# Optimization experiments

Measured on AMD Instinct MI355X. Metric: run time of the kernel, lower is better.

The kernel has to match this reference:

```python
import jax, jax.numpy as jnp
import numpy as np

S, I, IN_DIM, PROJ_DIM, OUT_DIM = 128, 384, 256, 32, 128
LN_EPS = 1e-5


def _layer_norm(x):
    # utils.normalize in OmegaFold: F.layer_norm over last dim, no affine params
    mu = jnp.mean(x, axis=-1, keepdims=True)
    var = jnp.var(x, axis=-1, keepdims=True)
    return (x - mu) * jax.lax.rsqrt(var + LN_EPS)


def setup_inputs() -> dict:
    key = jax.random.key(0)
    k0, k1, k2, k3 = jax.random.split(key, 4)
    node_repr = jax.random.normal(k0, (S, I, IN_DIM), dtype=jnp.float32)
    mask = (jax.random.uniform(k1, (S, I)) < 0.9).astype(jnp.float32)
    W_proj = jax.random.normal(k2, (IN_DIM, 2 * PROJ_DIM), dtype=jnp.float32) / np.sqrt(IN_DIM)
    b_proj = jnp.zeros((2 * PROJ_DIM,), dtype=jnp.float32)
    out_weights = jax.random.normal(k3, (PROJ_DIM, PROJ_DIM, OUT_DIM), dtype=jnp.float32) * 0.02
    out_bias = jnp.zeros((OUT_DIM,), dtype=jnp.float32)
    return {
        "node_repr": node_repr,
        "mask": mask,
        "W_proj": W_proj,
        "b_proj": b_proj,
        "out_weights": out_weights,
        "out_bias": out_bias,
    }


def reference(node_repr, mask, W_proj, b_proj, out_weights, out_bias):
    # LayerNorm (no affine) -> linear projection to 2*proj_dim
    x = _layer_norm(node_repr)                       # [s, i, in_dim]
    act = x @ W_proj + b_proj                        # [s, i, 2d]
    m = mask[..., None]                              # [s, i, 1]
    act = act * m
    # mask-pair counts: einsum('si,sj->ij')
    norm = jnp.einsum("si,sj->ij", mask, mask)[..., None]  # [i, j, 1]
    l = act[..., :PROJ_DIM]                          # [s, i, d]
    r = act[..., PROJ_DIM:]                          # [s, j, e]
    # outer-product mean over s, then contract (d,e)->f with the 3-tensor
    outer = jnp.einsum("sid,sje->ijde", l, r)        # [i, j, d, e]
    out = jnp.einsum("ijde,def->ijf", outer, out_weights) + out_bias  # [i, j, f]
    return out / (norm + 0.001)
```

## Files before the change

kernel.cpp:

```cpp
#include <hip/hip_runtime.h>

#define S_DIM 128
#define I_DIM 384
#define IN_DIM 256
#define PD 32
#define ODIM 128

typedef __attribute__((ext_vector_type(8))) __bf16 bf16x8;
typedef __attribute__((ext_vector_type(4))) float f32x4;

#define MFMA16(a, b, c) __builtin_amdgcn_mfma_f32_16x16x32_bf16((a), (b), (c), 0, 0, 0)

__device__ inline unsigned short f2bf(float f) {
    unsigned int u = __builtin_bit_cast(unsigned int, f);
    unsigned int r = (u + 0x7FFFu + ((u >> 16) & 1u)) >> 16;
    return (unsigned short)r;
}

__global__ void prep_cast(const float* __restrict__ Wp, const float* __restrict__ W2,
                          unsigned short* __restrict__ WpT, unsigned short* __restrict__ W2t) {
    int t = blockIdx.x * 256 + threadIdx.x;
    if (t < 64 * 256) {
        int f = t >> 8, k = t & 255;
        WpT[t] = f2bf(Wp[k * 64 + f]);
    }
    if (t < 128 * 1024) {
        int f = t >> 10, de = t & 1023;
        int e = de >> 5, d = de & 31;
        W2t[t] = f2bf(W2[(d * 32 + e) * 128 + f]);
    }
}

__global__ void norm_kernel(const float* __restrict__ mask, float* __restrict__ invn) {
    __shared__ float mi[S_DIM][16];
    __shared__ float mj[S_DIM][16];
    int t = threadIdx.x;
    int i0 = blockIdx.y * 16, j0 = blockIdx.x * 16;
    for (int p = 0; p < 8; ++p) {
        int s = p * 16 + (t >> 4);
        int c = t & 15;
        mi[s][c] = mask[s * I_DIM + i0 + c];
        mj[s][c] = mask[s * I_DIM + j0 + c];
    }
    __syncthreads();
    int ii = t >> 4, jj = t & 15;
    float acc = 0.f;
#pragma unroll 8
    for (int s = 0; s < S_DIM; ++s) acc += mi[s][ii] * mj[s][jj];
    invn[(i0 + ii) * I_DIM + (j0 + jj)] = 1.0f / (acc + 0.001f);
}

__global__ __launch_bounds__(256, 2) void ln_proj(const float* __restrict__ x,
                                                  const float* __restrict__ mask,
                                                  const float* __restrict__ bias,
                                                  const unsigned short* __restrict__ WpT_g,
                                                  unsigned short* __restrict__ lT,
                                                  unsigned short* __restrict__ rT) {
    __shared__ unsigned short xsh[64 * 264];
    __shared__ unsigned short wpT[64 * 264];
    int t = threadIdx.x;
    int w = t >> 6, lane = t & 63;
    int i = blockIdx.x >> 1;
    int s0 = (blockIdx.x & 1) * 64;

    {
        int f = t >> 2, kq = (t & 3) * 64;
#pragma unroll
        for (int p = 0; p < 8; ++p) {
            int k = kq + p * 8;
            *(uint4*)&wpT[f * 264 + k] = *(const uint4*)&WpT_g[f * 256 + k];
        }
    }

    float4 vbuf[4];
#pragma unroll
    for (int p = 0; p < 4; ++p)
        vbuf[p] = *(const float4*)(x + ((size_t)(s0 + w * 16 + p) * I_DIM + i) * IN_DIM + lane * 4);

    for (int it = 0; it < 16; ++it) {
        float4 v = vbuf[it & 3];
        if (it + 4 < 16)
            vbuf[it & 3] = *(const float4*)(x + ((size_t)(s0 + w * 16 + it + 4) * I_DIM + i) * IN_DIM + lane * 4);
        float s1 = v.x + v.y + v.z + v.w;
        float s2 = v.x * v.x + v.y * v.y + v.z * v.z + v.w * v.w;
#pragma unroll
        for (int off = 32; off >= 1; off >>= 1) {
            s1 += __shfl_xor(s1, off);
            s2 += __shfl_xor(s2, off);
        }
        float mu = s1 * (1.f / 256.f);
        float var = s2 * (1.f / 256.f) - mu * mu;
        float rs = rsqrtf(var + 1e-5f);
        unsigned int h0 = f2bf((v.x - mu) * rs);
        unsigned int h1 = f2bf((v.y - mu) * rs);
        unsigned int h2 = f2bf((v.z - mu) * rs);
        unsigned int h3 = f2bf((v.w - mu) * rs);
        uint2 pk;
        pk.x = h0 | (h1 << 16);
        pk.y = h2 | (h3 << 16);
        *(uint2*)&xsh[(w * 16 + it) * 264 + lane * 4] = pk;
    }
    __syncthreads();

    int l15 = lane & 15, q = lane >> 4;
    f32x4 acc[4];
#pragma unroll
    for (int nt = 0; nt < 4; ++nt) acc[nt] = (f32x4){0.f, 0.f, 0.f, 0.f};

    for (int k0 = 0; k0 < 256; k0 += 32) {
        bf16x8 a = *(bf16x8*)&xsh[(w * 16 + l15) * 264 + k0 + q * 8];
#pragma unroll
        for (int nt = 0; nt < 4; ++nt) {
            bf16x8 b = *(bf16x8*)&wpT[(nt * 16 + l15) * 264 + k0 + q * 8];
            acc[nt] = MFMA16(a, b, acc[nt]);
        }
    }

    float mval[4];
#pragma unroll
    for (int reg = 0; reg < 4; ++reg)
        mval[reg] = mask[(size_t)(s0 + w * 16 + q * 4 + reg) * I_DIM + i];

    __syncthreads();
    unsigned short* trsh = xsh;

#pragma unroll
    for (int nt = 0; nt < 4; ++nt) {
        int f = nt * 16 + l15;
        float bv = bias[f];
        unsigned int lo = (unsigned int)f2bf((acc[nt][0] + bv) * mval[0]) |
                          ((unsigned int)f2bf((acc[nt][1] + bv) * mval[1]) << 16);
        unsigned int hi = (unsigned int)f2bf((acc[nt][2] + bv) * mval[2]) |
                          ((unsigned int)f2bf((acc[nt][3] + bv) * mval[3]) << 16);
        uint2 pk; pk.x = lo; pk.y = hi;
        *(uint2*)&trsh[f * 72 + w * 16 + q * 4] = pk;
    }
    __syncthreads();

    {
        int fr = t >> 2, so = (t & 3) * 16;
        unsigned short* dst = ((fr < 32) ? lT : rT) + ((size_t)(i * 32 + (fr & 31)) * 128 + s0 + so);
        *(uint4*)dst = *(uint4*)&trsh[fr * 72 + so];
        *(uint4*)(dst + 8) = *(uint4*)&trsh[fr * 72 + so + 8];
    }
}

__global__ __launch_bounds__(256, 4) void outer_kernel(const unsigned short* __restrict__ lT,
                                                       const unsigned short* __restrict__ rT,
                                                       unsigned short* __restrict__ Gp,
                                                       int ib0) {
    __shared__ unsigned short sh[128 * 136];
    int t = threadIdx.x;
    int bx = blockIdx.x, by = blockIdx.y;
    int colL0 = (ib0 + by) * 128, colR0 = bx * 128;
    int w = t >> 6, lane = t & 63, l15 = lane & 15, q = lane >> 4;

    const unsigned short* lbase = lT + (size_t)(colL0 + w * 32 + l15) * 128 + q * 8;
    bf16x8 a0 = *(const bf16x8*)(lbase);
    bf16x8 a1 = *(const bf16x8*)(lbase + 16 * 128);

    {
        int m0 = t >> 3, c0 = (t & 7) * 8;
        const unsigned short* rbase = rT + (size_t)(colR0 + m0) * 128 + c0;
#pragma unroll
        for (int p = 0; p < 4; ++p) {
            *(uint4*)&sh[(m0 + p * 32) * 136 + c0] = *(const uint4*)(rbase + (size_t)p * 32 * 128);
            *(uint4*)&sh[(m0 + p * 32) * 136 + c0 + 64] = *(const uint4*)(rbase + (size_t)p * 32 * 128 + 64);
        }
    }
    __syncthreads();

    f32x4 acc[2][8];
#pragma unroll
    for (int mt = 0; mt < 2; ++mt)
#pragma unroll
        for (int nt = 0; nt < 8; ++nt) acc[mt][nt] = (f32x4){0.f, 0.f, 0.f, 0.f};

#pragma unroll
    for (int k0 = 0; k0 < 4; ++k0) {
        bf16x8 na0 = a0, na1 = a1;
        if (k0 < 3) {
            na0 = *(const bf16x8*)(lbase + (k0 + 1) * 32);
            na1 = *(const bf16x8*)(lbase + 16 * 128 + (k0 + 1) * 32);
        }
#pragma unroll
        for (int nt = 0; nt < 8; ++nt) {
            bf16x8 b = *(bf16x8*)&sh[(nt * 16 + l15) * 136 + k0 * 32 + q * 8];
            acc[0][nt] = MFMA16(a0, b, acc[0][nt]);
            acc[1][nt] = MFMA16(a1, b, acc[1][nt]);
        }
        a0 = na0; a1 = na1;
    }
    __syncthreads();

#pragma unroll
    for (int mt = 0; mt < 2; ++mt) {
        int rowb = w * 32 + mt * 16 + q * 4;
        int chnk = rowb >> 3;
        int win = rowb & 7;
#pragma unroll
        for (int nt = 0; nt < 8; ++nt) {
            int col = nt * 16 + l15;
            int cs = chnk ^ (col >> 5);
            unsigned int lo = (unsigned int)f2bf(acc[mt][nt][0]) | ((unsigned int)f2bf(acc[mt][nt][1]) << 16);
            unsigned int hi = (unsigned int)f2bf(acc[mt][nt][2]) | ((unsigned int)f2bf(acc[mt][nt][3]) << 16);
            uint2 pk; pk.x = lo; pk.y = hi;
            *(uint2*)&sh[col * 136 + cs * 8 + win] = pk;
        }
    }
    __syncthreads();

#pragma unroll
    for (int p8 = 0; p8 < 8; ++p8) {
        int g = p8 * 256 + t;
        int pair_loc = g >> 7;
        int c16 = g & 127;
        int i_loc = pair_loc >> 2, j_loc = pair_loc & 3;
        int e = c16 >> 2;
        int n = j_loc * 32 + e;
        int cs = (i_loc * 4 + (c16 & 3)) ^ j_loc;
        uint4 v = *(uint4*)&sh[n * 136 + cs * 8];
        size_t row = (size_t)(by * 4 + i_loc) * I_DIM + bx * 4 + j_loc;
        *(uint4*)&Gp[row * 1024 + (size_t)c16 * 8] = v;
    }
}

__global__ __launch_bounds__(256, 4) void contract_kernel(const unsigned short* __restrict__ Gp,
                                                          const unsigned short* __restrict__ W2t,
                                                          const float* __restrict__ invn,
                                                          const float* __restrict__ out_bias,
                                                          float* __restrict__ out,
                                                          int pair0) {
    __shared__ unsigned short Ash[2][64 * 40];
    int t = threadIdx.x;
    int w = t >> 6, lane = t & 63, l15 = lane & 15, q = lane >> 4;
    int p0 = blockIdx.x * 64;

    int sr = t >> 2, sc = (t & 3) * 8;
    const unsigned short* agp = Gp + (size_t)(p0 + sr) * 1024 + sc;
    *(uint4*)&Ash[0][sr * 40 + sc] = *(const uint4*)(agp);

    f32x4 acc[4][2];
#pragma unroll
    for (int mt = 0; mt < 4; ++mt) {
        acc[mt][0] = (f32x4){0.f, 0.f, 0.f, 0.f};
        acc[mt][1] = (f32x4){0.f, 0.f, 0.f, 0.f};
    }
    const unsigned short* wb0 = W2t + (size_t)(w * 32 + l15) * 1024 + q * 8;
    const unsigned short* wb1 = wb0 + 16 * 1024;

    bf16x8 b0c = *(const bf16x8*)(wb0);
    bf16x8 b1c = *(const bf16x8*)(wb1);
    __syncthreads();

    for (int k0 = 0; k0 < 32; ++k0) {
        int cur = k0 & 1;
        uint4 nxtA;
        bf16x8 b0n = b0c, b1n = b1c;
        if (k0 < 31) {
            nxtA = *(const uint4*)(agp + (k0 + 1) * 32);
            b0n = *(const bf16x8*)(wb0 + (k0 + 1) * 32);
            b1n = *(const bf16x8*)(wb1 + (k0 + 1) * 32);
        }
        bf16x8 a[4];
#pragma unroll
        for (int mt = 0; mt < 4; ++mt)
            a[mt] = *(bf16x8*)&Ash[cur][(mt * 16 + l15) * 40 + q * 8];
#pragma unroll
        for (int mt = 0; mt < 4; ++mt) {
            acc[mt][0] = MFMA16(a[mt], b0c, acc[mt][0]);
            acc[mt][1] = MFMA16(a[mt], b1c, acc[mt][1]);
        }
        if (k0 < 31) *(uint4*)&Ash[1 - cur][sr * 40 + sc] = nxtA;
        b0c = b0n; b1c = b1n;
        __syncthreads();
    }

#pragma unroll
    for (int u = 0; u < 2; ++u) {
        int f = w * 32 + u * 16 + l15;
        float bv = out_bias[f];
#pragma unroll
        for (int mt = 0; mt < 4; ++mt) {
#pragma unroll
            for (int reg = 0; reg < 4; ++reg) {
                int pl = pair0 + p0 + mt * 16 + q * 4 + reg;
                out[(size_t)pl * 128 + f] = (acc[mt][u][reg] + bv) * invn[pl];
            }
        }
    }
}

extern "C" void kernel_launch(void* const* d_in, const int* in_sizes, int n_in,
                              void* d_out, int out_size, void* d_ws, size_t ws_size,
                              hipStream_t stream) {
    const float* node = (const float*)d_in[0];
    const float* mask = (const float*)d_in[1];
    const float* Wp   = (const float*)d_in[2];
    const float* bp   = (const float*)d_in[3];
    const float* W2   = (const float*)d_in[4];
    const float* bo   = (const float*)d_in[5];
    float* out = (float*)d_out;

    char* ws = (char*)d_ws;
    unsigned short* lT  = (unsigned short*)(ws);
    unsigned short* rT  = (unsigned short*)(ws + 3145728);
    unsigned short* W2t = (unsigned short*)(ws + 6291456);
    unsigned short* WpT = (unsigned short*)(ws + 6553600);
    float*          inv = (float*)(ws + 6586368);
    unsigned short* Gp  = (unsigned short*)(ws + 8388608);

    int slab_i = 96;
    while (slab_i > 12 && 8388608ull + (size_t)slab_i * 384 * 1024 * 2 > ws_size) slab_i >>= 1;
    int nslab = 384 / slab_i;

    hipLaunchKernelGGL(prep_cast, dim3(512), dim3(256), 0, stream, Wp, W2, WpT, W2t);
    hipLaunchKernelGGL(norm_kernel, dim3(24, 24), dim3(256), 0, stream, mask, inv);
    hipLaunchKernelGGL(ln_proj, dim3(768), dim3(256), 0, stream, node, mask, bp, WpT, lT, rT);

    for (int s = 0; s < nslab; ++s) {
        hipLaunchKernelGGL(outer_kernel, dim3(96, slab_i / 4), dim3(256), 0, stream,
                           lT, rT, Gp, s * (slab_i / 4));
        hipLaunchKernelGGL(contract_kernel, dim3(slab_i * 384 / 64), dim3(256), 0, stream,
                           Gp, W2t, inv, bo, out, s * slab_i * I_DIM);
    }
}
```

Measured before the change: 332.0 us.

## Feed contract MFMA straight from global with reordered Gp and W2 layouts

```diff
diff --git a/kernel.cpp b/kernel.cpp
--- a/kernel.cpp
+++ b/kernel.cpp
@@ -18,16 +18,17 @@
 }
 
 __global__ void prep_cast(const float* __restrict__ Wp, const float* __restrict__ W2,
-                          unsigned short* __restrict__ WpT, unsigned short* __restrict__ W2t) {
+                          unsigned short* __restrict__ WpT, unsigned short* __restrict__ W2s) {
     int t = blockIdx.x * 256 + threadIdx.x;
     if (t < 64 * 256) {
         int f = t >> 8, k = t & 255;
         WpT[t] = f2bf(Wp[k * 64 + f]);
     }
     if (t < 128 * 1024) {
-        int f = t >> 10, de = t & 1023;
-        int e = de >> 5, d = de & 31;
-        W2t[t] = f2bf(W2[(d * 32 + e) * 128 + f]);
+        int j = t & 7, q = (t >> 3) & 3, f = (t >> 5) & 127, k0 = t >> 12;
+        int k = k0 * 32 + q * 8 + j;
+        int e = k >> 5, d = k & 31;
+        W2s[t] = f2bf(W2[(d * 32 + e) * 128 + f]);
     }
 }
 
@@ -195,17 +196,18 @@
 
 #pragma unroll
     for (int mt = 0; mt < 2; ++mt) {
-        int rowb = w * 32 + mt * 16 + q * 4;
-        int chnk = rowb >> 3;
-        int win = rowb & 7;
+        int rowbase = w * 32 + mt * 16;
+        int i_loc = rowbase >> 5;
+        int d = (rowbase & 31) + q * 4;
 #pragma unroll
         for (int nt = 0; nt < 8; ++nt) {
             int col = nt * 16 + l15;
-            int cs = chnk ^ (col >> 5);
+            int j_loc = col >> 5, e = col & 31;
+            int pair = i_loc * 4 + j_loc;
             unsigned int lo = (unsigned int)f2bf(acc[mt][nt][0]) | ((unsigned int)f2bf(acc[mt][nt][1]) << 16);
             unsigned int hi = (unsigned int)f2bf(acc[mt][nt][2]) | ((unsigned int)f2bf(acc[mt][nt][3]) << 16);
             uint2 pk; pk.x = lo; pk.y = hi;
-            *(uint2*)&sh[col * 136 + cs * 8 + win] = pk;
+            *(uint2*)&sh[pair * 1032 + e * 32 + d] = pk;
         }
     }
     __syncthreads();
@@ -215,30 +217,24 @@
         int g = p8 * 256 + t;
         int pair_loc = g >> 7;
         int c16 = g & 127;
-        int i_loc = pair_loc >> 2, j_loc = pair_loc & 3;
-        int e = c16 >> 2;
-        int n = j_loc * 32 + e;
-        int cs = (i_loc * 4 + (c16 & 3)) ^ j_loc;
-        uint4 v = *(uint4*)&sh[n * 136 + cs * 8];
-        size_t row = (size_t)(by * 4 + i_loc) * I_DIM + bx * 4 + j_loc;
+        uint4 v = *(uint4*)&sh[pair_loc * 1032 + c16 * 8];
+        size_t row = (size_t)(by * 4 + (pair_loc >> 2)) * I_DIM + bx * 4 + (pair_loc & 3);
         *(uint4*)&Gp[row * 1024 + (size_t)c16 * 8] = v;
     }
 }
 
 __global__ __launch_bounds__(256, 4) void contract_kernel(const unsigned short* __restrict__ Gp,
-                                                          const unsigned short* __restrict__ W2t,
+                                                          const unsigned short* __restrict__ W2s,
                                                           const float* __restrict__ invn,
                                                           const float* __restrict__ out_bias,
                                                           float* __restrict__ out,
                                                           int pair0) {
-    __shared__ unsigned short Ash[2][64 * 40];
     int t = threadIdx.x;
     int w = t >> 6, lane = t & 63, l15 = lane & 15, q = lane >> 4;
-    int p0 = blockIdx.x * 64;
-
-    int sr = t >> 2, sc = (t & 3) * 8;
-    const unsigned short* agp = Gp + (size_t)(p0 + sr) * 1024 + sc;
-    *(uint4*)&Ash[0][sr * 40 + sc] = *(const uint4*)(agp);
+    size_t p0 = (size_t)blockIdx.x * 64;
+
+    const unsigned short* a_base = Gp + (p0 + l15) * 1024 + q * 8;
+    const unsigned short* w_base = W2s + (w * 32 + l15) * 32 + q * 8;
 
     f32x4 acc[4][2];
 #pragma unroll
@@ -246,34 +242,40 @@
         acc[mt][0] = (f32x4){0.f, 0.f, 0.f, 0.f};
         acc[mt][1] = (f32x4){0.f, 0.f, 0.f, 0.f};
     }
-    const unsigned short* wb0 = W2t + (size_t)(w * 32 + l15) * 1024 + q * 8;
-    const unsigned short* wb1 = wb0 + 16 * 1024;
-
-    bf16x8 b0c = *(const bf16x8*)(wb0);
-    bf16x8 b1c = *(const bf16x8*)(wb1);
-    __syncthreads();
+
+    bf16x8 aC[4], aN[4], bC[2], bN[2];
+#pragma unroll
+    for (int mt = 0; mt < 4; ++mt) {
+        aC[mt] = *(const bf16x8*)(a_base + mt * 16384);
+        aN[mt] = *(const bf16x8*)(a_base + mt * 16384 + 32);
+    }
+    bC[0] = *(const bf16x8*)(w_base);
+    bC[1] = *(const bf16x8*)(w_base + 512);
+    bN[0] = *(const bf16x8*)(w_base + 4096);
+    bN[1] = *(const bf16x8*)(w_base + 4096 + 512);
 
     for (int k0 = 0; k0 < 32; ++k0) {
-        int cur = k0 & 1;
-        uint4 nxtA;
-        bf16x8 b0n = b0c, b1n = b1c;
-        if (k0 < 31) {
-            nxtA = *(const uint4*)(agp + (k0 + 1) * 32);
-            b0n = *(const bf16x8*)(wb0 + (k0 + 1) * 32);
-            b1n = *(const bf16x8*)(wb1 + (k0 + 1) * 32);
-        }
-        bf16x8 a[4];
-#pragma unroll
-        for (int mt = 0; mt < 4; ++mt)
-            a[mt] = *(bf16x8*)&Ash[cur][(mt * 16 + l15) * 40 + q * 8];
+        bf16x8 aP[4], bP[2];
+#pragma unroll
+        for (int mt = 0; mt < 4; ++mt) aP[mt] = aN[mt];
+        bP[0] = bN[0]; bP[1] = bN[1];
+        if (k0 + 2 < 32) {
+            int off = (k0 + 2) * 32;
+#pragma unroll
+            for (int mt = 0; mt < 4; ++mt)
+                aP[mt] = *(const bf16x8*)(a_base + mt * 16384 + off);
+            bP[0] = *(const bf16x8*)(w_base + (size_t)(k0 + 2) * 4096);
+            bP[1] = *(const bf16x8*)(w_base + (size_t)(k0 + 2) * 4096 + 512);
+        }
 #pragma unroll
         for (int mt = 0; mt < 4; ++mt) {
-            acc[mt][0] = MFMA16(a[mt], b0c, acc[mt][0]);
-            acc[mt][1] = MFMA16(a[mt], b1c, acc[mt][1]);
-        }
-        if (k0 < 31) *(uint4*)&Ash[1 - cur][sr * 40 + sc] = nxtA;
-        b0c = b0n; b1c = b1n;
-        __syncthreads();
+            acc[mt][0] = MFMA16(aC[mt], bC[0], acc[mt][0]);
+            acc[mt][1] = MFMA16(aC[mt], bC[1], acc[mt][1]);
+        }
+#pragma unroll
+        for (int mt = 0; mt < 4; ++mt) { aC[mt] = aN[mt]; aN[mt] = aP[mt]; }
+        bC[0] = bN[0]; bC[1] = bN[1];
+        bN[0] = bP[0]; bN[1] = bP[1];
     }
 
 #pragma unroll
@@ -284,8 +286,8 @@
         for (int mt = 0; mt < 4; ++mt) {
 #pragma unroll
             for (int reg = 0; reg < 4; ++reg) {
-                int pl = pair0 + p0 + mt * 16 + q * 4 + reg;
-                out[(size_t)pl * 128 + f] = (acc[mt][u][reg] + bv) * invn[pl];
+                size_t pl = (size_t)pair0 + p0 + mt * 16 + q * 4 + reg;
+                out[pl * 128 + f] = (acc[mt][u][reg] + bv) * invn[pl];
             }
         }
     }
@@ -305,23 +307,23 @@
     char* ws = (char*)d_ws;
     unsigned short* lT  = (unsigned short*)(ws);
     unsigned short* rT  = (unsigned short*)(ws + 3145728);
-    unsigned short* W2t = (unsigned short*)(ws + 6291456);
+    unsigned short* W2s = (unsigned short*)(ws + 6291456);
     unsigned short* WpT = (unsigned short*)(ws + 6553600);
     float*          inv = (float*)(ws + 6586368);
     unsigned short* Gp  = (unsigned short*)(ws + 8388608);
 
-    int slab_i = 96;
+    int slab_i = 192;
     while (slab_i > 12 && 8388608ull + (size_t)slab_i * 384 * 1024 * 2 > ws_size) slab_i >>= 1;
     int nslab = 384 / slab_i;
 
-    hipLaunchKernelGGL(prep_cast, dim3(512), dim3(256), 0, stream, Wp, W2, WpT, W2t);
+    hipLaunchKernelGGL(prep_cast, dim3(512), dim3(256), 0, stream, Wp, W2, WpT, W2s);
     hipLaunchKernelGGL(norm_kernel, dim3(24, 24), dim3(256), 0, stream, mask, inv);
     hipLaunchKernelGGL(ln_proj, dim3(768), dim3(256), 0, stream, node, mask, bp, WpT, lT, rT);
 
     for (int s = 0; s < nslab; ++s) {
         hipLaunchKernelGGL(outer_kernel, dim3(96, slab_i / 4), dim3(256), 0, stream,
                            lT, rT, Gp, s * (slab_i / 4));
-        hipLaunchKernelGGL(contract_kernel, dim3(slab_i * 384 / 64), dim3(256), 0, stream,
-                           Gp, W2t, inv, bo, out, s * slab_i * I_DIM);
-    }
-}
+        hipLaunchKernelGGL(contract_kernel, dim3(slab_i * 6), dim3(256), 0, stream,
+                           Gp, W2s, inv, bo, out, s * slab_i * I_DIM);
+    }
+}
```

After: 408.6 us. 1.23x slower.
